# Kernel tuning notes

Hardware: AMD Instinct MI355X
Metric: run time of the kernel (lower is better)

## Reference

```python
import jax, jax.numpy as jnp
import numpy as np

EPS = 1e-5

def _act_quant(x):
    # per-row int8 quant-dequant over last dim
    scale = 127.0 / jnp.clip(jnp.max(jnp.abs(x), axis=-1, keepdims=True), EPS)
    return jnp.clip(jnp.round(x * scale), -128.0, 127.0) / scale

def _weight_quant(w):
    # per-tensor ternary quant-dequant
    scale = 1.0 / jnp.clip(jnp.mean(jnp.abs(w)), EPS)
    return jnp.clip(jnp.round(w * scale), -1.0, 1.0) / scale

def setup_inputs() -> dict:
    key = jax.random.key(0)
    k1, k2 = jax.random.split(key)
    x = jax.random.normal(k1, (1024, 3, 160, 160), dtype=jnp.float32)
    W = jax.random.normal(k2, (8, 160 * 160 * 3), dtype=jnp.float32) * 0.02
    return {"x": x, "W": W}

def reference(x, W):
    B = x.shape[0]
    xf = x.reshape(B, -1)  # [B, 76800]
    # STE: forward uses quantized values, gradient passes through
    xq = xf + jax.lax.stop_gradient(_act_quant(xf) - xf)
    wq = W + jax.lax.stop_gradient(_weight_quant(W) - W)
    y = jnp.einsum('bi,oi->bo', xq, wq)  # [B, 8]
    return jax.nn.softmax(y, axis=1)
```

## Files before the change

kernel.cpp:

```cpp
#include <hip/hip_runtime.h>


constexpr int B_ROWS  = 1024;
constexpr int I_ELEMS = 76800;
constexpr int I_F4    = 19200;
constexpr int O_OUT   = 8;
constexpr int W_N     = O_OUT * I_ELEMS;
constexpr int W_F4    = W_N / 4;
constexpr float EPS   = 1e-5f;

__global__ __launch_bounds__(256) void k_wabs_sum(const float* __restrict__ W,
                                                  double* __restrict__ wsum) {
  int tid = blockIdx.x * blockDim.x + threadIdx.x;
  int stride = gridDim.x * blockDim.x;
  float s = 0.f;
  for (int f = tid; f < W_F4; f += stride) {
    float4 v = reinterpret_cast<const float4*>(W)[f];
    s += fabsf(v.x) + fabsf(v.y) + fabsf(v.z) + fabsf(v.w);
  }
  double d = (double)s;
  #pragma unroll
  for (int off = 32; off; off >>= 1) d += __shfl_xor(d, off);
  __shared__ double lds[4];
  int lane = threadIdx.x & 63;
  int wv   = threadIdx.x >> 6;
  if (lane == 0) lds[wv] = d;
  __syncthreads();
  if (threadIdx.x == 0) atomicAdd(wsum, lds[0] + lds[1] + lds[2] + lds[3]);
}

__global__ __launch_bounds__(256) void k_pack(const float* __restrict__ W,
                                              const double* __restrict__ wsum,
                                              unsigned int* __restrict__ codes) {
  int tid = blockIdx.x * blockDim.x + threadIdx.x;
  if (tid >= W_F4) return;
  float meanc = fmaxf((float)(*wsum * (1.0 / (double)W_N)), EPS);
  float sw = 1.f / meanc;
  float4 v = reinterpret_cast<const float4*>(W)[tid];
  int b0 = (int)fminf(fmaxf(rintf(v.x * sw), -1.f), 1.f);
  int b1 = (int)fminf(fmaxf(rintf(v.y * sw), -1.f), 1.f);
  int b2 = (int)fminf(fmaxf(rintf(v.z * sw), -1.f), 1.f);
  int b3 = (int)fminf(fmaxf(rintf(v.w * sw), -1.f), 1.f);
  codes[tid] = (unsigned)(b0 & 0xff)        | ((unsigned)(b1 & 0xff) << 8) |
               ((unsigned)(b2 & 0xff) << 16) | ((unsigned)(b3 & 0xff) << 24);
}

__global__ __launch_bounds__(512) void k_main(const float* __restrict__ X,
                                              const unsigned int* __restrict__ codes,
                                              const double* __restrict__ wsum,
                                              float* __restrict__ out) {
  __shared__ float red[8];
  __shared__ float racc[8][8];
  const int t    = threadIdx.x;
  const int lane = t & 63;
  const int wv   = t >> 6;
  const float meanc = fmaxf((float)(*wsum * (1.0 / (double)W_N)), EPS);

  #pragma unroll 1
  for (int rr = 0; rr < 2; ++rr) {
    const int row = (blockIdx.x << 1) + rr;
    const float4* __restrict__ xrow =
        reinterpret_cast<const float4*>(X + (size_t)row * I_ELEMS);

    float m = 0.f;
    #pragma unroll 4
    for (int k = 0; k < 37; ++k) {
      float4 v = xrow[t + (k << 9)];
      m = fmaxf(m, fmaxf(fmaxf(fabsf(v.x), fabsf(v.y)),
                         fmaxf(fabsf(v.z), fabsf(v.w))));
    }
    if (t < 256) {
      float4 v = xrow[t + 18944];
      m = fmaxf(m, fmaxf(fmaxf(fabsf(v.x), fabsf(v.y)),
                         fmaxf(fabsf(v.z), fabsf(v.w))));
    }
    #pragma unroll
    for (int off = 32; off; off >>= 1) m = fmaxf(m, __shfl_xor(m, off));
    if (lane == 0) red[wv] = m;
    __syncthreads();
    float rowmax = red[0];
    #pragma unroll
    for (int i = 1; i < 8; ++i) rowmax = fmaxf(rowmax, red[i]);
    const float maxc = fmaxf(rowmax, EPS);
    const float sx = 127.f / maxc;

    float acc[8];
    #pragma unroll
    for (int o = 0; o < O_OUT; ++o) acc[o] = 0.f;

    auto body = [&](int f) {
      float4 v = xrow[f];
      float q0 = fminf(fmaxf(rintf(v.x * sx), -128.f), 127.f);
      float q1 = fminf(fmaxf(rintf(v.y * sx), -128.f), 127.f);
      float q2 = fminf(fmaxf(rintf(v.z * sx), -128.f), 127.f);
      float q3 = fminf(fmaxf(rintf(v.w * sx), -128.f), 127.f);
      #pragma unroll
      for (int o = 0; o < O_OUT; ++o) {
        unsigned w4 = codes[o * I_F4 + f];
        acc[o] += q0 * (float)((int)(w4 << 24) >> 24);
        acc[o] += q1 * (float)((int)(w4 << 16) >> 24);
        acc[o] += q2 * (float)((int)(w4 <<  8) >> 24);
        acc[o] += q3 * (float)((int)w4 >> 24);
      }
    };

    if (t < 256) body(t + 18944);
    #pragma unroll 2
    for (int k = 36; k >= 0; --k) body(t + (k << 9));

    #pragma unroll
    for (int o = 0; o < O_OUT; ++o) {
      float a = acc[o];
      #pragma unroll
      for (int off = 32; off; off >>= 1) a += __shfl_xor(a, off);
      if (lane == 0) racc[wv][o] = a;
    }
    __syncthreads();

    if (t == 0) {
      const float fin = maxc * meanc * (1.f / 127.f);
      float y[8];
      #pragma unroll
      for (int o = 0; o < O_OUT; ++o)
        y[o] = (racc[0][o] + racc[1][o] + racc[2][o] + racc[3][o] +
                racc[4][o] + racc[5][o] + racc[6][o] + racc[7][o]) * fin;
      float mx = y[0];
      #pragma unroll
      for (int o = 1; o < O_OUT; ++o) mx = fmaxf(mx, y[o]);
      float e[8], s = 0.f;
      #pragma unroll
      for (int o = 0; o < O_OUT; ++o) { e[o] = expf(y[o] - mx); s += e[o]; }
      float inv = 1.f / s;
      #pragma unroll
      for (int o = 0; o < O_OUT; ++o) out[row * O_OUT + o] = e[o] * inv;
    }
    __syncthreads();
  }
}

extern "C" void kernel_launch(void* const* d_in, const int* in_sizes, int n_in,
                              void* d_out, int out_size, void* d_ws, size_t ws_size,
                              hipStream_t stream) {
  const float* X = (const float*)d_in[0];
  const float* W = (const float*)d_in[1];
  float* out = (float*)d_out;

  double* wsum = (double*)d_ws;
  unsigned int* codes = (unsigned int*)((char*)d_ws + 64);

  hipMemsetAsync(d_ws, 0, 8, stream);
  k_wabs_sum<<<256, 256, 0, stream>>>(W, wsum);
  k_pack<<<(W_F4 + 255) / 256, 256, 0, stream>>>(W, wsum, codes);
  k_main<<<B_ROWS / 2, 512, 0, stream>>>(X, codes, wsum, out);
}
```

Measured before the change: 481.0 us.

## Register-cache rows with next-row prefetch and interleave ternary codes by column

Each 768-thread block now processes four rows. A thread keeps its 25 float4 slices of the current row in registers, so the row max and the quantized dot product share one global read. While computing the current row, it issues the loads for the next row. The packed weight codes are stored interleaved by input position, so all eight outputs' codes for one float4 come in two uint4 loads instead of eight scattered loads. The aim is to turn a latency-bound streaming pass into a deeply pipelined one, at the cost of heavy register pressure and fewer blocks on the grid.

```diff
diff --git a/kernel.cpp b/kernel.cpp
--- a/kernel.cpp
+++ b/kernel.cpp
@@ -8,6 +8,10 @@
 constexpr int W_N     = O_OUT * I_ELEMS;
 constexpr int W_F4    = W_N / 4;
 constexpr float EPS   = 1e-5f;
+
+constexpr int TPB = 768;
+constexpr int F4T = 25;
+constexpr int RPB = 4;
 
 __global__ __launch_bounds__(256) void k_wabs_sum(const float* __restrict__ W,
                                                   double* __restrict__ wsum) {
@@ -31,7 +35,7 @@
 
 __global__ __launch_bounds__(256) void k_pack(const float* __restrict__ W,
                                               const double* __restrict__ wsum,
-                                              unsigned int* __restrict__ codes) {
+                                              unsigned int* __restrict__ cT) {
   int tid = blockIdx.x * blockDim.x + threadIdx.x;
   if (tid >= W_F4) return;
   float meanc = fmaxf((float)(*wsum * (1.0 / (double)W_N)), EPS);
@@ -41,36 +45,38 @@
   int b1 = (int)fminf(fmaxf(rintf(v.y * sw), -1.f), 1.f);
   int b2 = (int)fminf(fmaxf(rintf(v.z * sw), -1.f), 1.f);
   int b3 = (int)fminf(fmaxf(rintf(v.w * sw), -1.f), 1.f);
-  codes[tid] = (unsigned)(b0 & 0xff)        | ((unsigned)(b1 & 0xff) << 8) |
-               ((unsigned)(b2 & 0xff) << 16) | ((unsigned)(b3 & 0xff) << 24);
+  unsigned packed = (unsigned)(b0 & 0xff)        | ((unsigned)(b1 & 0xff) << 8) |
+                    ((unsigned)(b2 & 0xff) << 16) | ((unsigned)(b3 & 0xff) << 24);
+  int o = tid / I_F4;
+  int f = tid - o * I_F4;
+  cT[(size_t)f * 8 + o] = packed;
 }
 
-__global__ __launch_bounds__(512) void k_main(const float* __restrict__ X,
-                                              const unsigned int* __restrict__ codes,
+__global__ __launch_bounds__(TPB) void k_main(const float* __restrict__ X,
+                                              const unsigned int* __restrict__ cT,
                                               const double* __restrict__ wsum,
                                               float* __restrict__ out) {
-  __shared__ float red[8];
-  __shared__ float racc[8][8];
+  __shared__ float red[12];
+  __shared__ float racc[12][8];
   const int t    = threadIdx.x;
   const int lane = t & 63;
   const int wv   = t >> 6;
   const float meanc = fmaxf((float)(*wsum * (1.0 / (double)W_N)), EPS);
+  const int row0 = blockIdx.x * RPB;
+
+  float4 d[F4T];
+  {
+    const float4* xr = reinterpret_cast<const float4*>(X) + (size_t)row0 * I_F4;
+    #pragma unroll
+    for (int j = 0; j < F4T; ++j) d[j] = xr[t + j * TPB];
+  }
 
   #pragma unroll 1
-  for (int rr = 0; rr < 2; ++rr) {
-    const int row = (blockIdx.x << 1) + rr;
-    const float4* __restrict__ xrow =
-        reinterpret_cast<const float4*>(X + (size_t)row * I_ELEMS);
-
+  for (int r = 0; r < RPB; ++r) {
     float m = 0.f;
-    #pragma unroll 4
-    for (int k = 0; k < 37; ++k) {
-      float4 v = xrow[t + (k << 9)];
-      m = fmaxf(m, fmaxf(fmaxf(fabsf(v.x), fabsf(v.y)),
-                         fmaxf(fabsf(v.z), fabsf(v.w))));
-    }
-    if (t < 256) {
-      float4 v = xrow[t + 18944];
+    #pragma unroll
+    for (int j = 0; j < F4T; ++j) {
+      float4 v = d[j];
       m = fmaxf(m, fmaxf(fmaxf(fabsf(v.x), fabsf(v.y)),
                          fmaxf(fabsf(v.z), fabsf(v.w))));
     }
@@ -80,7 +86,7 @@
     __syncthreads();
     float rowmax = red[0];
     #pragma unroll
-    for (int i = 1; i < 8; ++i) rowmax = fmaxf(rowmax, red[i]);
+    for (int i = 1; i < 12; ++i) rowmax = fmaxf(rowmax, red[i]);
     const float maxc = fmaxf(rowmax, EPS);
     const float sx = 127.f / maxc;
 
@@ -88,25 +94,56 @@
     #pragma unroll
     for (int o = 0; o < O_OUT; ++o) acc[o] = 0.f;
 
-    auto body = [&](int f) {
-      float4 v = xrow[f];
+    const bool pre = (r + 1 < RPB);
+    const int nrow = pre ? (row0 + r + 1) : (row0 + r);
+    const float4* xn = reinterpret_cast<const float4*>(X) + (size_t)nrow * I_F4;
+
+    #pragma unroll
+    for (int j = 0; j < F4T; ++j) {
+      const int f = t + j * TPB;
+      float4 v = d[j];
+      if (pre) d[j] = xn[f];
       float q0 = fminf(fmaxf(rintf(v.x * sx), -128.f), 127.f);
       float q1 = fminf(fmaxf(rintf(v.y * sx), -128.f), 127.f);
       float q2 = fminf(fmaxf(rintf(v.z * sx), -128.f), 127.f);
       float q3 = fminf(fmaxf(rintf(v.w * sx), -128.f), 127.f);
-      #pragma unroll
-      for (int o = 0; o < O_OUT; ++o) {
-        unsigned w4 = codes[o * I_F4 + f];
-        acc[o] += q0 * (float)((int)(w4 << 24) >> 24);
-        acc[o] += q1 * (float)((int)(w4 << 16) >> 24);
-        acc[o] += q2 * (float)((int)(w4 <<  8) >> 24);
-        acc[o] += q3 * (float)((int)w4 >> 24);
-      }
-    };
-
-    if (t < 256) body(t + 18944);
-    #pragma unroll 2
-    for (int k = 36; k >= 0; --k) body(t + (k << 9));
+      const uint4* cp = reinterpret_cast<const uint4*>(cT + ((size_t)f << 3));
+      uint4 c0 = cp[0];
+      uint4 c1 = cp[1];
+      unsigned cw;
+      cw = c0.x; acc[0] += q0 * (float)((int)(cw << 24) >> 24) +
+                           q1 * (float)((int)(cw << 16) >> 24) +
+                           q2 * (float)((int)(cw <<  8) >> 24) +
+                           q3 * (float)((int)cw >> 24);
+      cw = c0.y; acc[1] += q0 * (float)((int)(cw << 24) >> 24) +
+                           q1 * (float)((int)(cw << 16) >> 24) +
+                           q2 * (float)((int)(cw <<  8) >> 24) +
+                           q3 * (float)((int)cw >> 24);
+      cw = c0.z; acc[2] += q0 * (float)((int)(cw << 24) >> 24) +
+                           q1 * (float)((int)(cw << 16) >> 24) +
+                           q2 * (float)((int)(cw <<  8) >> 24) +
+                           q3 * (float)((int)cw >> 24);
+      cw = c0.w; acc[3] += q0 * (float)((int)(cw << 24) >> 24) +
+                           q1 * (float)((int)(cw << 16) >> 24) +
+                           q2 * (float)((int)(cw <<  8) >> 24) +
+                           q3 * (float)((int)cw >> 24);
+      cw = c1.x; acc[4] += q0 * (float)((int)(cw << 24) >> 24) +
+                           q1 * (float)((int)(cw << 16) >> 24) +
+                           q2 * (float)((int)(cw <<  8) >> 24) +
+                           q3 * (float)((int)cw >> 24);
+      cw = c1.y; acc[5] += q0 * (float)((int)(cw << 24) >> 24) +
+                           q1 * (float)((int)(cw << 16) >> 24) +
+                           q2 * (float)((int)(cw <<  8) >> 24) +
+                           q3 * (float)((int)cw >> 24);
+      cw = c1.z; acc[6] += q0 * (float)((int)(cw << 24) >> 24) +
+                           q1 * (float)((int)(cw << 16) >> 24) +
+                           q2 * (float)((int)(cw <<  8) >> 24) +
+                           q3 * (float)((int)cw >> 24);
+      cw = c1.w; acc[7] += q0 * (float)((int)(cw << 24) >> 24) +
+                           q1 * (float)((int)(cw << 16) >> 24) +
+                           q2 * (float)((int)(cw <<  8) >> 24) +
+                           q3 * (float)((int)cw >> 24);
+    }
 
     #pragma unroll
     for (int o = 0; o < O_OUT; ++o) {
@@ -121,9 +158,12 @@
       const float fin = maxc * meanc * (1.f / 127.f);
       float y[8];
       #pragma unroll
-      for (int o = 0; o < O_OUT; ++o)
-        y[o] = (racc[0][o] + racc[1][o] + racc[2][o] + racc[3][o] +
-                racc[4][o] + racc[5][o] + racc[6][o] + racc[7][o]) * fin;
+      for (int o = 0; o < O_OUT; ++o) {
+        float s = 0.f;
+        #pragma unroll
+        for (int w = 0; w < 12; ++w) s += racc[w][o];
+        y[o] = s * fin;
+      }
       float mx = y[0];
       #pragma unroll
       for (int o = 1; o < O_OUT; ++o) mx = fmaxf(mx, y[o]);
@@ -132,9 +172,8 @@
       for (int o = 0; o < O_OUT; ++o) { e[o] = expf(y[o] - mx); s += e[o]; }
       float inv = 1.f / s;
       #pragma unroll
-      for (int o = 0; o < O_OUT; ++o) out[row * O_OUT + o] = e[o] * inv;
+      for (int o = 0; o < O_OUT; ++o) out[(row0 + r) * O_OUT + o] = e[o] * inv;
     }
-    __syncthreads();
   }
 }
 
@@ -146,10 +185,10 @@
   float* out = (float*)d_out;
 
   double* wsum = (double*)d_ws;
-  unsigned int* codes = (unsigned int*)((char*)d_ws + 64);
+  unsigned int* cT = (unsigned int*)((char*)d_ws + 64);
 
   hipMemsetAsync(d_ws, 0, 8, stream);
   k_wabs_sum<<<256, 256, 0, stream>>>(W, wsum);
-  k_pack<<<(W_F4 + 255) / 256, 256, 0, stream>>>(W, wsum, codes);
-  k_main<<<B_ROWS / 2, 512, 0, stream>>>(X, codes, wsum, out);
+  k_pack<<<(W_F4 + 255) / 256, 256, 0, stream>>>(W, wsum, cT);
+  k_main<<<B_ROWS / RPB, TPB, 0, stream>>>(X, cT, wsum, out);
 }
```

Measured after the change: 1.736 ms. 261% more time.
